# Optimization experiments

Measured on AMD Instinct MI355X. Metric: run time of the kernel, lower is better.

The kernel has to match this reference:

```python
import jax, jax.numpy as jnp
import numpy as np

TEMPERATURE = 8.0  # sqrt(d_k) with d_k = 64
MASK_FILL = -65504.0  # fp16 min, as in the original


def setup_inputs() -> dict:
    key = jax.random.key(0)
    kq, kk, kv, km = jax.random.split(key, 4)
    BH, L, D = 16, 2048, 64
    q = jax.random.normal(kq, (BH, L, D), dtype=jnp.float32)
    k = jax.random.normal(kk, (BH, L, D), dtype=jnp.float32)
    v = jax.random.normal(kv, (BH, L, D), dtype=jnp.float32)
    mask = jax.random.randint(km, (BH, L, L), 0, 2).astype(jnp.bool_)
    return {"q": q, "k": k, "v": v, "mask": mask}


def reference(q, k, v, mask):
    # attn = q @ k^T / temperature, masked_fill, softmax over last dim
    attn = jnp.einsum("bqd,bkd->bqk", q, k) / TEMPERATURE
    attn = jnp.where(mask, MASK_FILL, attn)
    attn = jax.nn.softmax(attn, axis=2)
    # dropout with p=0.0 is identity (eval-mode reference)
    output = jnp.einsum("bqk,bkd->bqd", attn, v)
    return (output, attn)
```

## Files before the change

kernel.cpp:

```cpp
#include <hip/hip_runtime.h>

#define BH 16
#define L 2048
#define D 64
#define QB 64
#define KB 64
#define NKT (L / KB)
#define SCALE 0.125f
#define MASK_FILL -65504.0f

typedef __bf16 bf16x8 __attribute__((ext_vector_type(8)));
typedef float f32x4 __attribute__((ext_vector_type(4)));

__device__ __forceinline__ unsigned f2bf(float f) {
    union { float f; unsigned u; } x; x.f = f;
    return (x.u + 0x7FFFu + ((x.u >> 16) & 1u)) >> 16;
}
__device__ __forceinline__ float bf2f(unsigned short h) {
    union { unsigned u; float f; } x; x.u = ((unsigned)h) << 16;
    return x.f;
}

extern "C" __global__ __launch_bounds__(256)
void prep(const float* __restrict__ k, const float* __restrict__ v,
          const int* __restrict__ mask,
          uint4* __restrict__ wsK, uint4* __restrict__ wsVt,
          unsigned* __restrict__ wsM2)
{
    __shared__ float sT[64 * 68];
    const int b = blockIdx.x;
    const int t = threadIdx.x;

    if (b < 2048) {
        size_t row0 = (size_t)b * 16;
        int lane = t & 63, w4 = t >> 6;
        const int* src = mask + row0 * L;
        unsigned* dst = wsM2 + row0 * 64;
        for (int rr = 0; rr < 4; ++rr) {
            int r = w4 * 4 + rr;
            unsigned word = 0;
            #pragma unroll
            for (int kt = 0; kt < 32; ++kt) {
                int val = __builtin_nontemporal_load(src + (size_t)r * L + kt * 64 + lane);
                word |= (val != 0 ? 1u : 0u) << kt;
            }
            dst[(size_t)r * 64 + lane] = word;
        }
    } else if (b < 3072) {
        int idx = (b - 2048) * 256 + t;
        int c   = idx & 7;
        int key = (idx >> 3) & (L - 1);
        int bh  = idx >> 14;
        const float4* src = (const float4*)(k + ((size_t)(bh * L + key) * D + c * 8));
        float4 a = src[0], bb = src[1];
        uint4 o;
        o.x = f2bf(a.x)  | (f2bf(a.y)  << 16);
        o.y = f2bf(a.z)  | (f2bf(a.w)  << 16);
        o.z = f2bf(bb.x) | (f2bf(bb.y) << 16);
        o.w = f2bf(bb.z) | (f2bf(bb.w) << 16);
        wsK[(size_t)(bh * L + key) * 8 + (c ^ (key & 7))] = o;
    } else {
        int bb = b - 3072;
        int bh = bb >> 5, kt = bb & 31;
        const float4* src = (const float4*)(v + ((size_t)bh * L + kt * 64) * D);
        #pragma unroll
        for (int i = 0; i < 4; ++i) {
            int i4 = i * 256 + t;
            int key = i4 >> 4, c4 = i4 & 15;
            float4 val = src[i4];
            *(float4*)&sT[key * 68 + c4 * 4] = val;
        }
        __syncthreads();
        int d = t >> 2, cg = t & 3;
        #pragma unroll
        for (int j = 0; j < 2; ++j) {
            int c = cg + j * 4;
            unsigned pk[4];
            #pragma unroll
            for (int e = 0; e < 4; ++e) {
                float x0 = sT[(c * 8 + e * 2    ) * 68 + d];
                float x1 = sT[(c * 8 + e * 2 + 1) * 68 + d];
                pk[e] = f2bf(x0) | (f2bf(x1) << 16);
            }
            wsVt[((size_t)(bh * 32 + kt) * 64 + d) * 8 + (c ^ (d & 7))] =
                make_uint4(pk[0], pk[1], pk[2], pk[3]);
        }
    }
}


struct KF { bf16x8 f[8]; };

extern "C" __global__ __launch_bounds__(256, 2)
void sdpa_main(const float* __restrict__ q, const uint4* __restrict__ gKall,
               const uint4* __restrict__ gVall, const unsigned* __restrict__ wsM2,
               float* __restrict__ out, float* __restrict__ attn)
{
    __shared__ unsigned short sP[4][2][16 * 72];

    const int tid = threadIdx.x, lane = tid & 63, w = tid >> 6;
    const int quad = lane >> 4, l15 = lane & 15;
    const int p = blockIdx.x, bh = p & 15, qb = p >> 4;
    const int row0 = qb * QB + w * 16;

    const uint4* gK = gKall + (size_t)bh * L * 8;
    const uint4* gV = gVall + (size_t)bh * L * 8;

    const float* Qp = q + (size_t)(bh * L + row0 + l15) * D + quad * 8;
    float4 qv0 = *(const float4*)(Qp);
    float4 qv1 = *(const float4*)(Qp + 4);
    float4 qv2 = *(const float4*)(Qp + 32);
    float4 qv3 = *(const float4*)(Qp + 36);
    union { bf16x8 v; unsigned short s[8]; } qa0u, qa1u;
    qa0u.s[0] = f2bf(qv0.x * SCALE); qa0u.s[1] = f2bf(qv0.y * SCALE);
    qa0u.s[2] = f2bf(qv0.z * SCALE); qa0u.s[3] = f2bf(qv0.w * SCALE);
    qa0u.s[4] = f2bf(qv1.x * SCALE); qa0u.s[5] = f2bf(qv1.y * SCALE);
    qa0u.s[6] = f2bf(qv1.z * SCALE); qa0u.s[7] = f2bf(qv1.w * SCALE);
    qa1u.s[0] = f2bf(qv2.x * SCALE); qa1u.s[1] = f2bf(qv2.y * SCALE);
    qa1u.s[2] = f2bf(qv2.z * SCALE); qa1u.s[3] = f2bf(qv2.w * SCALE);
    qa1u.s[4] = f2bf(qv3.x * SCALE); qa1u.s[5] = f2bf(qv3.y * SCALE);
    qa1u.s[6] = f2bf(qv3.z * SCALE); qa1u.s[7] = f2bf(qv3.w * SCALE);
    const bf16x8 qa0 = qa0u.v, qa1 = qa1u.v;

    const int s7 = l15 & 7;
    int off[8];
    #pragma unroll
    for (int nt = 0; nt < 4; ++nt) {
        off[nt * 2    ] = (nt * 16 + l15) * 8 + ((quad    ) ^ s7);
        off[nt * 2 + 1] = (nt * 16 + l15) * 8 + ((quad + 4) ^ s7);
    }

    auto loadT = [&](const uint4* base, KF& d) {
        #pragma unroll
        for (int i = 0; i < 8; ++i) d.f[i] = *(const bf16x8*)(base + off[i]);
    };

    const unsigned* Mp = wsM2 + ((size_t)(bh * L) + row0 + quad * 4) * 64 + l15;
    unsigned mb[16];
    #pragma unroll
    for (int r = 0; r < 4; ++r)
        #pragma unroll
        for (int nt = 0; nt < 4; ++nt)
            mb[r * 4 + nt] = Mp[r * 64 + nt * 16];

    float lsum[4] = {0.f, 0.f, 0.f, 0.f};

    KF ka, kb;
    loadT(gK, ka);
    loadT(gK + 512, kb);

    for (int kt = 0; kt < NKT; kt += 2) {
        {
            f32x4 acc[4];
            #pragma unroll
            for (int nt = 0; nt < 4; ++nt) {
                acc[nt] = (f32x4){0.f, 0.f, 0.f, 0.f};
                acc[nt] = __builtin_amdgcn_mfma_f32_16x16x32_bf16(qa0, ka.f[nt*2  ], acc[nt], 0, 0, 0);
                acc[nt] = __builtin_amdgcn_mfma_f32_16x16x32_bf16(qa1, ka.f[nt*2+1], acc[nt], 0, 0, 0);
            }
            if (kt + 2 < NKT) loadT(gK + (size_t)(kt + 2) * 512, ka);
            #pragma unroll
            for (int nt = 0; nt < 4; ++nt)
                #pragma unroll
                for (int r = 0; r < 4; ++r) {
                    float e = __expf(acc[nt][r]);
                    lsum[r] += ((mb[r * 4 + nt] >> kt) & 1u) ? 0.f : e;
                }
        }
        {
            f32x4 acc[4];
            #pragma unroll
            for (int nt = 0; nt < 4; ++nt) {
                acc[nt] = (f32x4){0.f, 0.f, 0.f, 0.f};
                acc[nt] = __builtin_amdgcn_mfma_f32_16x16x32_bf16(qa0, kb.f[nt*2  ], acc[nt], 0, 0, 0);
                acc[nt] = __builtin_amdgcn_mfma_f32_16x16x32_bf16(qa1, kb.f[nt*2+1], acc[nt], 0, 0, 0);
            }
            if (kt + 3 < NKT) loadT(gK + (size_t)(kt + 3) * 512, kb);
            #pragma unroll
            for (int nt = 0; nt < 4; ++nt)
                #pragma unroll
                for (int r = 0; r < 4; ++r) {
                    float e = __expf(acc[nt][r]);
                    lsum[r] += ((mb[r * 4 + nt] >> (kt + 1)) & 1u) ? 0.f : e;
                }
        }
    }

    #pragma unroll
    for (int o = 1; o < 16; o <<= 1)
        #pragma unroll
        for (int r = 0; r < 4; ++r) lsum[r] += __shfl_xor(lsum[r], o, 64);
    float rinv[4];
    #pragma unroll
    for (int r = 0; r < 4; ++r) rinv[r] = 1.0f / lsum[r];

    f32x4 oacc[4];
    #pragma unroll
    for (int d = 0; d < 4; ++d) oacc[d] = (f32x4){0.f, 0.f, 0.f, 0.f};
    float* Ab = attn + ((size_t)bh * L + row0) * L;

    unsigned short* sw0 = &sP[w][0][0];
    unsigned short* sw1 = &sP[w][1][0];

    KF kc, kn, vc;
    loadT(gK, kc);

    for (int kt = 0; kt < NKT; kt += 2) {
        {
            loadT(gV + (size_t)kt * 512, vc);
            f32x4 acc[4];
            #pragma unroll
            for (int nt = 0; nt < 4; ++nt) {
                acc[nt] = (f32x4){0.f, 0.f, 0.f, 0.f};
                acc[nt] = __builtin_amdgcn_mfma_f32_16x16x32_bf16(qa0, kc.f[nt*2  ], acc[nt], 0, 0, 0);
                acc[nt] = __builtin_amdgcn_mfma_f32_16x16x32_bf16(qa1, kc.f[nt*2+1], acc[nt], 0, 0, 0);
            }
            loadT(gK + (size_t)(kt + 1) * 512, kn);
            #pragma unroll
            for (int nt = 0; nt < 4; ++nt)
                #pragma unroll
                for (int r = 0; r < 4; ++r) {
                    float e = __expf(acc[nt][r]);
                    float pr = (((mb[r * 4 + nt] >> kt) & 1u) ? 0.f : e) * rinv[r];
                    const int row = quad * 4 + r;
                    Ab[(size_t)row * L + kt * 64 + nt * 16 + l15] = pr;
                    sw0[row * 72 + nt * 16 + l15] = (unsigned short)f2bf(pr);
                }
            const bf16x8 pa0 = *(const bf16x8*)&sw0[l15 * 72 + quad * 8];
            const bf16x8 pa1 = *(const bf16x8*)&sw0[l15 * 72 + quad * 8 + 32];
            #pragma unroll
            for (int d = 0; d < 4; ++d) {
                oacc[d] = __builtin_amdgcn_mfma_f32_16x16x32_bf16(pa0, vc.f[d*2  ], oacc[d], 0, 0, 0);
                oacc[d] = __builtin_amdgcn_mfma_f32_16x16x32_bf16(pa1, vc.f[d*2+1], oacc[d], 0, 0, 0);
            }
        }
        {
            loadT(gV + (size_t)(kt + 1) * 512, vc);
            f32x4 acc[4];
            #pragma unroll
            for (int nt = 0; nt < 4; ++nt) {
                acc[nt] = (f32x4){0.f, 0.f, 0.f, 0.f};
                acc[nt] = __builtin_amdgcn_mfma_f32_16x16x32_bf16(qa0, kn.f[nt*2  ], acc[nt], 0, 0, 0);
                acc[nt] = __builtin_amdgcn_mfma_f32_16x16x32_bf16(qa1, kn.f[nt*2+1], acc[nt], 0, 0, 0);
            }
            if (kt + 2 < NKT) loadT(gK + (size_t)(kt + 2) * 512, kc);
            #pragma unroll
            for (int nt = 0; nt < 4; ++nt)
                #pragma unroll
                for (int r = 0; r < 4; ++r) {
                    float e = __expf(acc[nt][r]);
                    float pr = (((mb[r * 4 + nt] >> (kt + 1)) & 1u) ? 0.f : e) * rinv[r];
                    const int row = quad * 4 + r;
                    Ab[(size_t)row * L + (kt + 1) * 64 + nt * 16 + l15] = pr;
                    sw1[row * 72 + nt * 16 + l15] = (unsigned short)f2bf(pr);
                }
            const bf16x8 pa0 = *(const bf16x8*)&sw1[l15 * 72 + quad * 8];
            const bf16x8 pa1 = *(const bf16x8*)&sw1[l15 * 72 + quad * 8 + 32];
            #pragma unroll
            for (int d = 0; d < 4; ++d) {
                oacc[d] = __builtin_amdgcn_mfma_f32_16x16x32_bf16(pa0, vc.f[d*2  ], oacc[d], 0, 0, 0);
                oacc[d] = __builtin_amdgcn_mfma_f32_16x16x32_bf16(pa1, vc.f[d*2+1], oacc[d], 0, 0, 0);
            }
        }
    }

    float* Ob = out + ((size_t)bh * L + row0) * D;
    #pragma unroll
    for (int d = 0; d < 4; ++d)
        #pragma unroll
        for (int r = 0; r < 4; ++r)
            Ob[(size_t)(quad * 4 + r) * D + d * 16 + l15] = oacc[d][r];
}


extern "C" __global__ __launch_bounds__(256, 2)
void sdpa_kernel(const float* __restrict__ q, const float* __restrict__ k,
                 const float* __restrict__ v, const int* __restrict__ mask,
                 float* __restrict__ out, float* __restrict__ attn)
{
    __shared__ unsigned short fQ[64 * 72];
    __shared__ unsigned short fK[64 * 72];
    __shared__ unsigned short fVt[64 * 72];
    __shared__ unsigned short fP[64 * 72];
    __shared__ unsigned long long fM[64 * 33];

    const int tid  = threadIdx.x;
    const int lane = tid & 63;
    const int w    = tid >> 6;
    const int quad = lane >> 4;
    const int l15  = lane & 15;

    const int p  = blockIdx.x;
    const int bh = p & (BH - 1);
    const int qb = p >> 4;
    const int q0 = qb * 64;

    const size_t base = (size_t)bh * L * D;
    const float* Qb = q + base + (size_t)q0 * D;
    const float* Kb = k + base;
    const float* Vb = v + base;
    const int*   Mb = mask + (size_t)bh * L * L + (size_t)q0 * L;
    float*       Ab = attn + (size_t)bh * L * L + (size_t)q0 * L;
    float*       Ob = out  + base + (size_t)q0 * D;

    {
        const float2* Qs = (const float2*)Qb;
        for (int i = 0; i < 8; ++i) {
            int idx = i * 256 + tid;
            int row = idx >> 5, d2 = idx & 31;
            float2 val = Qs[idx];
            unsigned pk = f2bf(val.x) | (f2bf(val.y) << 16);
            *(unsigned*)&fQ[row * 72 + d2 * 2] = pk;
        }
    }
    for (int rr = 0; rr < 16; ++rr) {
        int row = w * 16 + rr;
        const int4* Ms = (const int4*)(Mb + (size_t)row * L);
        for (int it = 0; it < 8; ++it) {
            int4 mv = Ms[it * 64 + lane];
            unsigned long long b0 = __ballot(mv.x != 0);
            unsigned long long b1 = __ballot(mv.y != 0);
            unsigned long long b2 = __ballot(mv.z != 0);
            unsigned long long b3 = __ballot(mv.w != 0);
            if (lane == 0) {
                unsigned long long* dst = &fM[row * 33 + it * 4];
                dst[0] = b0; dst[1] = b1; dst[2] = b2; dst[3] = b3;
            }
        }
    }
    __syncthreads();

    const int qrow = w * 16 + l15;
    bf16x8 qa0 = *(const bf16x8*)&fQ[qrow * 72 + quad * 8];
    bf16x8 qa1 = *(const bf16x8*)&fQ[qrow * 72 + quad * 8 + 32];

    float lsum[4] = {0.f, 0.f, 0.f, 0.f};
    for (int kt = 0; kt < 32; ++kt) {
        const int k0 = kt * 64;
        __syncthreads();
        {
            const float2* Ks = (const float2*)(Kb + (size_t)k0 * D);
            for (int i = 0; i < 8; ++i) {
                int idx = i * 256 + tid;
                int row = idx >> 5, d2 = idx & 31;
                float2 val = Ks[idx];
                unsigned pk = f2bf(val.x) | (f2bf(val.y) << 16);
                *(unsigned*)&fK[row * 72 + d2 * 2] = pk;
            }
        }
        __syncthreads();
        f32x4 acc[4];
        for (int nt = 0; nt < 4; ++nt) {
            bf16x8 b0 = *(const bf16x8*)&fK[(nt * 16 + l15) * 72 + quad * 8];
            bf16x8 b1 = *(const bf16x8*)&fK[(nt * 16 + l15) * 72 + quad * 8 + 32];
            f32x4 c = {0.f, 0.f, 0.f, 0.f};
            c = __builtin_amdgcn_mfma_f32_16x16x32_bf16(qa0, b0, c, 0, 0, 0);
            c = __builtin_amdgcn_mfma_f32_16x16x32_bf16(qa1, b1, c, 0, 0, 0);
            acc[nt] = c;
        }
        const int widx = (k0 >> 8) * 4 + (lane & 3);
        const int bsh0 = (k0 >> 2) + (l15 >> 2);
        for (int r = 0; r < 4; ++r) {
            int row = w * 16 + quad * 4 + r;
            unsigned long long mwv = fM[row * 33 + widx];
            float s = 0.f;
            for (int nt = 0; nt < 4; ++nt) {
                float val = acc[nt][r] * SCALE;
                int bit = (int)((mwv >> ((bsh0 + nt * 4) & 63)) & 1ull);
                val = bit ? MASK_FILL : val;
                s += __expf(val);
            }
            lsum[r] += s;
        }
    }
    for (int off = 1; off < 16; off <<= 1)
        for (int r = 0; r < 4; ++r) lsum[r] += __shfl_xor(lsum[r], off, 64);
    float rinv[4];
    for (int r = 0; r < 4; ++r) rinv[r] = 1.0f / lsum[r];

    f32x4 oacc[4];
    for (int nt = 0; nt < 4; ++nt) oacc[nt] = (f32x4){0.f, 0.f, 0.f, 0.f};

    for (int kt = 0; kt < 32; ++kt) {
        const int k0 = kt * 64;
        __syncthreads();
        {
            const float2* Ks = (const float2*)(Kb + (size_t)k0 * D);
            for (int i = 0; i < 8; ++i) {
                int idx = i * 256 + tid;
                int row = idx >> 5, d2 = idx & 31;
                float2 val = Ks[idx];
                unsigned pk = f2bf(val.x) | (f2bf(val.y) << 16);
                *(unsigned*)&fK[row * 72 + d2 * 2] = pk;
            }
        }
        {
            unsigned pk[8];
            for (int jj = 0; jj < 16; ++jj) {
                float val = Vb[(size_t)(k0 + w * 16 + jj) * D + lane];
                unsigned bv = f2bf(val);
                if (jj & 1) pk[jj >> 1] |= bv << 16;
                else        pk[jj >> 1]  = bv;
            }
            uint4* dst = (uint4*)&fVt[lane * 72 + w * 16];
            dst[0] = make_uint4(pk[0], pk[1], pk[2], pk[3]);
            dst[1] = make_uint4(pk[4], pk[5], pk[6], pk[7]);
        }
        __syncthreads();
        f32x4 acc[4];
        for (int nt = 0; nt < 4; ++nt) {
            bf16x8 b0 = *(const bf16x8*)&fK[(nt * 16 + l15) * 72 + quad * 8];
            bf16x8 b1 = *(const bf16x8*)&fK[(nt * 16 + l15) * 72 + quad * 8 + 32];
            f32x4 c = {0.f, 0.f, 0.f, 0.f};
            c = __builtin_amdgcn_mfma_f32_16x16x32_bf16(qa0, b0, c, 0, 0, 0);
            c = __builtin_amdgcn_mfma_f32_16x16x32_bf16(qa1, b1, c, 0, 0, 0);
            acc[nt] = c;
        }
        const int widx = (k0 >> 8) * 4 + (lane & 3);
        const int bsh0 = (k0 >> 2) + (l15 >> 2);
        for (int r = 0; r < 4; ++r) {
            int row = w * 16 + quad * 4 + r;
            unsigned long long mwv = fM[row * 33 + widx];
            for (int nt = 0; nt < 4; ++nt) {
                float val = acc[nt][r] * SCALE;
                int bit = (int)((mwv >> ((bsh0 + nt * 4) & 63)) & 1ull);
                val = bit ? MASK_FILL : val;
                float pr = __expf(val) * rinv[r];
                fP[row * 72 + nt * 16 + l15] = (unsigned short)f2bf(pr);
            }
        }
        for (int it = 0; it < 4; ++it) {
            int row = w * 16 + it * 4 + quad;
            unsigned long long pv = *(const unsigned long long*)&fP[row * 72 + l15 * 4];
            float4 o;
            o.x = bf2f((unsigned short)(pv         & 0xFFFF));
            o.y = bf2f((unsigned short)((pv >> 16) & 0xFFFF));
            o.z = bf2f((unsigned short)((pv >> 32) & 0xFFFF));
            o.w = bf2f((unsigned short)((pv >> 48) & 0xFFFF));
            *(float4*)&Ab[(size_t)row * L + k0 + l15 * 4] = o;
        }
        {
            bf16x8 pa0 = *(const bf16x8*)&fP[qrow * 72 + quad * 8];
            bf16x8 pa1 = *(const bf16x8*)&fP[qrow * 72 + quad * 8 + 32];
            for (int nt = 0; nt < 4; ++nt) {
                bf16x8 vb0 = *(const bf16x8*)&fVt[(nt * 16 + l15) * 72 + quad * 8];
                bf16x8 vb1 = *(const bf16x8*)&fVt[(nt * 16 + l15) * 72 + quad * 8 + 32];
                oacc[nt] = __builtin_amdgcn_mfma_f32_16x16x32_bf16(pa0, vb0, oacc[nt], 0, 0, 0);
                oacc[nt] = __builtin_amdgcn_mfma_f32_16x16x32_bf16(pa1, vb1, oacc[nt], 0, 0, 0);
            }
        }
    }
    for (int nt = 0; nt < 4; ++nt)
        for (int r = 0; r < 4; ++r)
            Ob[(size_t)(w * 16 + quad * 4 + r) * D + nt * 16 + l15] = oacc[nt][r];
}


extern "C" void kernel_launch(void* const* d_in, const int* in_sizes, int n_in,
                              void* d_out, int out_size, void* d_ws, size_t ws_size,
                              hipStream_t stream)
{
    const float* q    = (const float*)d_in[0];
    const float* k    = (const float*)d_in[1];
    const float* v    = (const float*)d_in[2];
    const int*   mask = (const int*)d_in[3];
    float* out  = (float*)d_out;
    float* attn = out + (size_t)BH * L * D;

    const size_t WS_K  = 0;
    const size_t WS_VT = (size_t)BH * L * D * 2;
    const size_t WS_M  = WS_VT + (size_t)BH * L * D * 2;
    const size_t NEED  = WS_M + (size_t)BH * L * 64 * 4;

    if (ws_size >= NEED) {
        uint4* wsK  = (uint4*)((char*)d_ws + WS_K);
        uint4* wsVt = (uint4*)((char*)d_ws + WS_VT);
        unsigned* wsM2 = (unsigned*)((char*)d_ws + WS_M);
        hipLaunchKernelGGL(prep, dim3(3584), dim3(256), 0, stream,
                           k, v, mask, wsK, wsVt, wsM2);
        hipLaunchKernelGGL(sdpa_main, dim3(BH * (L / QB)), dim3(256), 0, stream,
                           q, (const uint4*)wsK, (const uint4*)wsVt, wsM2, out, attn);
    } else {
        hipLaunchKernelGGL(sdpa_kernel, dim3(BH * (L / 64)), dim3(256), 0, stream,
                           q, k, v, mask, out, attn);
    }
}
```

Measured before the change: 506.7 us.

## Fuse mask bit-packing into main kernel via async global-to-LDS staging

Removes the mask-packing phase from the prep kernel. The main attention kernel now streams raw int mask tiles into shared memory with global_load_lds, triple-buffered per wave, and builds the per-row bitmasks during the first (row-sum) pass. The goal is to drop a separate pass that reads the whole mask and writes a packed workspace, and to overlap the mask reads with the QK MFMA work. The trade-offs are extra LDS use, which may limit occupancy, and a hand-coded vmcnt wait whose correctness depends on how many loads are in flight.

```diff
diff --git a/kernel.cpp b/kernel.cpp
--- a/kernel.cpp
+++ b/kernel.cpp
@@ -23,31 +23,14 @@
 
 extern "C" __global__ __launch_bounds__(256)
 void prep(const float* __restrict__ k, const float* __restrict__ v,
-          const int* __restrict__ mask,
-          uint4* __restrict__ wsK, uint4* __restrict__ wsVt,
-          unsigned* __restrict__ wsM2)
+          uint4* __restrict__ wsK, uint4* __restrict__ wsVt)
 {
     __shared__ float sT[64 * 68];
     const int b = blockIdx.x;
     const int t = threadIdx.x;
 
-    if (b < 2048) {
-        size_t row0 = (size_t)b * 16;
-        int lane = t & 63, w4 = t >> 6;
-        const int* src = mask + row0 * L;
-        unsigned* dst = wsM2 + row0 * 64;
-        for (int rr = 0; rr < 4; ++rr) {
-            int r = w4 * 4 + rr;
-            unsigned word = 0;
-            #pragma unroll
-            for (int kt = 0; kt < 32; ++kt) {
-                int val = __builtin_nontemporal_load(src + (size_t)r * L + kt * 64 + lane);
-                word |= (val != 0 ? 1u : 0u) << kt;
-            }
-            dst[(size_t)r * 64 + lane] = word;
-        }
-    } else if (b < 3072) {
-        int idx = (b - 2048) * 256 + t;
+    if (b < 1024) {
+        int idx = b * 256 + t;
         int c   = idx & 7;
         int key = (idx >> 3) & (L - 1);
         int bh  = idx >> 14;
@@ -60,7 +43,7 @@
         o.w = f2bf(bb.z) | (f2bf(bb.w) << 16);
         wsK[(size_t)(bh * L + key) * 8 + (c ^ (key & 7))] = o;
     } else {
-        int bb = b - 3072;
+        int bb = b - 1024;
         int bh = bb >> 5, kt = bb & 31;
         const float4* src = (const float4*)(v + ((size_t)bh * L + kt * 64) * D);
         #pragma unroll
@@ -93,9 +76,10 @@
 
 extern "C" __global__ __launch_bounds__(256, 2)
 void sdpa_main(const float* __restrict__ q, const uint4* __restrict__ gKall,
-               const uint4* __restrict__ gVall, const unsigned* __restrict__ wsM2,
+               const uint4* __restrict__ gVall, const int* __restrict__ mask,
                float* __restrict__ out, float* __restrict__ attn)
 {
+    __shared__ unsigned sM[4][3][16 * 68];
     __shared__ unsigned short sP[4][2][16 * 72];
 
     const int tid = threadIdx.x, lane = tid & 63, w = tid >> 6;
@@ -135,87 +119,90 @@
         for (int i = 0; i < 8; ++i) d.f[i] = *(const bf16x8*)(base + off[i]);
     };
 
-    const unsigned* Mp = wsM2 + ((size_t)(bh * L) + row0 + quad * 4) * 64 + l15;
+    const int* Mraw = mask + ((size_t)bh * L + row0) * L + lane;
+
+    auto stageM = [&](int kt, unsigned* buf) {
+        const int* src = Mraw + kt * 64;
+        #pragma unroll
+        for (int rr = 0; rr < 16; ++rr)
+            __builtin_amdgcn_global_load_lds(
+                (const __attribute__((address_space(1))) unsigned int*)(src + (size_t)rr * L),
+                (__attribute__((address_space(3))) unsigned int*)(buf + rr * 68), 4, 0, 0);
+    };
+
     unsigned mb[16];
     #pragma unroll
-    for (int r = 0; r < 4; ++r)
+    for (int i = 0; i < 16; ++i) mb[i] = 0u;
+
+    float lsum[4] = {0.f, 0.f, 0.f, 0.f};
+
+    unsigned* mbuf0 = &sM[w][0][0];
+    unsigned* mbuf1 = &sM[w][1][0];
+    unsigned* mbuf2 = &sM[w][2][0];
+    stageM(0, mbuf0); stageM(1, mbuf1); stageM(2, mbuf2);
+
+    KF kc, kn;
+    loadT(gK, kc);
+
+    for (int kt = 0; kt < NKT; ++kt) {
+        if (kt + 1 < NKT) loadT(gK + (size_t)(kt + 1) * 512, kn);
+
+        f32x4 acc[4];
+        #pragma unroll
+        for (int nt = 0; nt < 4; ++nt) {
+            acc[nt] = (f32x4){0.f, 0.f, 0.f, 0.f};
+            acc[nt] = __builtin_amdgcn_mfma_f32_16x16x32_bf16(qa0, kc.f[nt*2  ], acc[nt], 0, 0, 0);
+            acc[nt] = __builtin_amdgcn_mfma_f32_16x16x32_bf16(qa1, kc.f[nt*2+1], acc[nt], 0, 0, 0);
+        }
+
+        asm volatile("s_waitcnt vmcnt(32)" ::: "memory");
+
         #pragma unroll
         for (int nt = 0; nt < 4; ++nt)
-            mb[r * 4 + nt] = Mp[r * 64 + nt * 16];
-
-    float lsum[4] = {0.f, 0.f, 0.f, 0.f};
-
-    KF ka, kb;
-    loadT(gK, ka);
-    loadT(gK + 512, kb);
+            #pragma unroll
+            for (int r = 0; r < 4; ++r) {
+                unsigned mv = mbuf0[(quad * 4 + r) * 68 + nt * 16 + l15];
+                unsigned bit = mv ? 1u : 0u;
+                mb[r * 4 + nt] |= bit << kt;
+                float e = __expf(acc[nt][r]);
+                lsum[r] += bit ? 0.f : e;
+            }
+
+        if (kt + 3 < NKT) stageM(kt + 3, mbuf0);
+        unsigned* tmp = mbuf0; mbuf0 = mbuf1; mbuf1 = mbuf2; mbuf2 = tmp;
+        if (kt + 1 < NKT) kc = kn;
+    }
+
+    #pragma unroll
+    for (int o = 1; o < 16; o <<= 1)
+        #pragma unroll
+        for (int r = 0; r < 4; ++r) lsum[r] += __shfl_xor(lsum[r], o, 64);
+    float rinv[4];
+    #pragma unroll
+    for (int r = 0; r < 4; ++r) rinv[r] = 1.0f / lsum[r];
+
+    f32x4 oacc[4];
+    #pragma unroll
+    for (int d = 0; d < 4; ++d) oacc[d] = (f32x4){0.f, 0.f, 0.f, 0.f};
+    float* Ab = attn + ((size_t)bh * L + row0) * L;
+
+    unsigned short* sw0 = &sP[w][0][0];
+    unsigned short* sw1 = &sP[w][1][0];
+
+    KF kc2, kn2, vc;
+    loadT(gK, kc2);
 
     for (int kt = 0; kt < NKT; kt += 2) {
         {
+            loadT(gV + (size_t)kt * 512, vc);
             f32x4 acc[4];
             #pragma unroll
             for (int nt = 0; nt < 4; ++nt) {
                 acc[nt] = (f32x4){0.f, 0.f, 0.f, 0.f};
-                acc[nt] = __builtin_amdgcn_mfma_f32_16x16x32_bf16(qa0, ka.f[nt*2  ], acc[nt], 0, 0, 0);
-                acc[nt] = __builtin_amdgcn_mfma_f32_16x16x32_bf16(qa1, ka.f[nt*2+1], acc[nt], 0, 0, 0);
-            }
-            if (kt + 2 < NKT) loadT(gK + (size_t)(kt + 2) * 512, ka);
-            #pragma unroll
-            for (int nt = 0; nt < 4; ++nt)
-                #pragma unroll
-                for (int r = 0; r < 4; ++r) {
-                    float e = __expf(acc[nt][r]);
-                    lsum[r] += ((mb[r * 4 + nt] >> kt) & 1u) ? 0.f : e;
-                }
-        }
-        {
-            f32x4 acc[4];
-            #pragma unroll
-            for (int nt = 0; nt < 4; ++nt) {
-                acc[nt] = (f32x4){0.f, 0.f, 0.f, 0.f};
-                acc[nt] = __builtin_amdgcn_mfma_f32_16x16x32_bf16(qa0, kb.f[nt*2  ], acc[nt], 0, 0, 0);
-                acc[nt] = __builtin_amdgcn_mfma_f32_16x16x32_bf16(qa1, kb.f[nt*2+1], acc[nt], 0, 0, 0);
-            }
-            if (kt + 3 < NKT) loadT(gK + (size_t)(kt + 3) * 512, kb);
-            #pragma unroll
-            for (int nt = 0; nt < 4; ++nt)
-                #pragma unroll
-                for (int r = 0; r < 4; ++r) {
-                    float e = __expf(acc[nt][r]);
-                    lsum[r] += ((mb[r * 4 + nt] >> (kt + 1)) & 1u) ? 0.f : e;
-                }
-        }
-    }
-
-    #pragma unroll
-    for (int o = 1; o < 16; o <<= 1)
-        #pragma unroll
-        for (int r = 0; r < 4; ++r) lsum[r] += __shfl_xor(lsum[r], o, 64);
-    float rinv[4];
-    #pragma unroll
-    for (int r = 0; r < 4; ++r) rinv[r] = 1.0f / lsum[r];
-
-    f32x4 oacc[4];
-    #pragma unroll
-    for (int d = 0; d < 4; ++d) oacc[d] = (f32x4){0.f, 0.f, 0.f, 0.f};
-    float* Ab = attn + ((size_t)bh * L + row0) * L;
-
-    unsigned short* sw0 = &sP[w][0][0];
-    unsigned short* sw1 = &sP[w][1][0];
-
-    KF kc, kn, vc;
-    loadT(gK, kc);
-
-    for (int kt = 0; kt < NKT; kt += 2) {
-        {
-            loadT(gV + (size_t)kt * 512, vc);
-            f32x4 acc[4];
-            #pragma unroll
-            for (int nt = 0; nt < 4; ++nt) {
-                acc[nt] = (f32x4){0.f, 0.f, 0.f, 0.f};
-                acc[nt] = __builtin_amdgcn_mfma_f32_16x16x32_bf16(qa0, kc.f[nt*2  ], acc[nt], 0, 0, 0);
-                acc[nt] = __builtin_amdgcn_mfma_f32_16x16x32_bf16(qa1, kc.f[nt*2+1], acc[nt], 0, 0, 0);
-            }
-            loadT(gK + (size_t)(kt + 1) * 512, kn);
+                acc[nt] = __builtin_amdgcn_mfma_f32_16x16x32_bf16(qa0, kc2.f[nt*2  ], acc[nt], 0, 0, 0);
+                acc[nt] = __builtin_amdgcn_mfma_f32_16x16x32_bf16(qa1, kc2.f[nt*2+1], acc[nt], 0, 0, 0);
+            }
+            loadT(gK + (size_t)(kt + 1) * 512, kn2);
             #pragma unroll
             for (int nt = 0; nt < 4; ++nt)
                 #pragma unroll
@@ -240,10 +227,10 @@
             #pragma unroll
             for (int nt = 0; nt < 4; ++nt) {
                 acc[nt] = (f32x4){0.f, 0.f, 0.f, 0.f};
-                acc[nt] = __builtin_amdgcn_mfma_f32_16x16x32_bf16(qa0, kn.f[nt*2  ], acc[nt], 0, 0, 0);
-                acc[nt] = __builtin_amdgcn_mfma_f32_16x16x32_bf16(qa1, kn.f[nt*2+1], acc[nt], 0, 0, 0);
-            }
-            if (kt + 2 < NKT) loadT(gK + (size_t)(kt + 2) * 512, kc);
+                acc[nt] = __builtin_amdgcn_mfma_f32_16x16x32_bf16(qa0, kn2.f[nt*2  ], acc[nt], 0, 0, 0);
+                acc[nt] = __builtin_amdgcn_mfma_f32_16x16x32_bf16(qa1, kn2.f[nt*2+1], acc[nt], 0, 0, 0);
+            }
+            if (kt + 2 < NKT) loadT(gK + (size_t)(kt + 2) * 512, kc2);
             #pragma unroll
             for (int nt = 0; nt < 4; ++nt)
                 #pragma unroll
@@ -469,17 +456,15 @@
 
     const size_t WS_K  = 0;
     const size_t WS_VT = (size_t)BH * L * D * 2;
-    const size_t WS_M  = WS_VT + (size_t)BH * L * D * 2;
-    const size_t NEED  = WS_M + (size_t)BH * L * 64 * 4;
+    const size_t NEED  = WS_VT + (size_t)BH * L * D * 2;
 
     if (ws_size >= NEED) {
         uint4* wsK  = (uint4*)((char*)d_ws + WS_K);
         uint4* wsVt = (uint4*)((char*)d_ws + WS_VT);
-        unsigned* wsM2 = (unsigned*)((char*)d_ws + WS_M);
-        hipLaunchKernelGGL(prep, dim3(3584), dim3(256), 0, stream,
-                           k, v, mask, wsK, wsVt, wsM2);
+        hipLaunchKernelGGL(prep, dim3(1536), dim3(256), 0, stream,
+                           k, v, wsK, wsVt);
         hipLaunchKernelGGL(sdpa_main, dim3(BH * (L / QB)), dim3(256), 0, stream,
-                           q, (const uint4*)wsK, (const uint4*)wsVt, wsM2, out, attn);
+                           q, (const uint4*)wsK, (const uint4*)wsVt, mask, out, attn);
     } else {
         hipLaunchKernelGGL(sdpa_kernel, dim3(BH * (L / 64)), dim3(256), 0, stream,
                            q, k, v, mask, out, attn);
```

Measured after the change: 582.7 us. +15.0%, slower.

## Split key range across wave pairs and halve query block per workgroup

Applied to the files above, without the earlier changes.

Each workgroup now covers 32 query rows instead of 64. Pairs of waves split the key tiles in half, combine their partial row sums and output accumulators through shared memory, and use two block barriers to do so. Occupancy is raised to 4 blocks per SM and twice as many blocks are launched, giving more parallelism and latency hiding. In exchange there is extra shared-memory reduction traffic and register pressure under the tighter launch bound, and each K/V tile is reloaded by more blocks.

```diff
diff --git a/kernel.cpp b/kernel.cpp
--- a/kernel.cpp
+++ b/kernel.cpp
@@ -3,7 +3,7 @@
 #define BH 16
 #define L 2048
 #define D 64
-#define QB 64
+#define QB 32
 #define KB 64
 #define NKT (L / KB)
 #define SCALE 0.125f
@@ -91,17 +91,22 @@
 
 struct KF { bf16x8 f[8]; };
 
-extern "C" __global__ __launch_bounds__(256, 2)
+extern "C" __global__ __launch_bounds__(256, 4)
 void sdpa_main(const float* __restrict__ q, const uint4* __restrict__ gKall,
                const uint4* __restrict__ gVall, const unsigned* __restrict__ wsM2,
                float* __restrict__ out, float* __restrict__ attn)
 {
     __shared__ unsigned short sP[4][2][16 * 72];
+    __shared__ float sPart[4][16];
+    __shared__ float sO[2][16][68];
 
     const int tid = threadIdx.x, lane = tid & 63, w = tid >> 6;
+    const int rg = w >> 1, h = w & 1;
     const int quad = lane >> 4, l15 = lane & 15;
     const int p = blockIdx.x, bh = p & 15, qb = p >> 4;
-    const int row0 = qb * QB + w * 16;
+    const int row0 = qb * QB + rg * 16;
+    const int kt0 = h * (NKT / 2);
+    const int ktE = kt0 + (NKT / 2);
 
     const uint4* gK = gKall + (size_t)bh * L * 8;
     const uint4* gV = gVall + (size_t)bh * L * 8;
@@ -146,10 +151,10 @@
     float lsum[4] = {0.f, 0.f, 0.f, 0.f};
 
     KF ka, kb;
-    loadT(gK, ka);
-    loadT(gK + 512, kb);
-
-    for (int kt = 0; kt < NKT; kt += 2) {
+    loadT(gK + (size_t)kt0 * 512, ka);
+    loadT(gK + (size_t)(kt0 + 1) * 512, kb);
+
+    for (int kt = kt0; kt < ktE; kt += 2) {
         {
             f32x4 acc[4];
             #pragma unroll
@@ -158,7 +163,7 @@
                 acc[nt] = __builtin_amdgcn_mfma_f32_16x16x32_bf16(qa0, ka.f[nt*2  ], acc[nt], 0, 0, 0);
                 acc[nt] = __builtin_amdgcn_mfma_f32_16x16x32_bf16(qa1, ka.f[nt*2+1], acc[nt], 0, 0, 0);
             }
-            if (kt + 2 < NKT) loadT(gK + (size_t)(kt + 2) * 512, ka);
+            if (kt + 2 < ktE) loadT(gK + (size_t)(kt + 2) * 512, ka);
             #pragma unroll
             for (int nt = 0; nt < 4; ++nt)
                 #pragma unroll
@@ -175,7 +180,7 @@
                 acc[nt] = __builtin_amdgcn_mfma_f32_16x16x32_bf16(qa0, kb.f[nt*2  ], acc[nt], 0, 0, 0);
                 acc[nt] = __builtin_amdgcn_mfma_f32_16x16x32_bf16(qa1, kb.f[nt*2+1], acc[nt], 0, 0, 0);
             }
-            if (kt + 3 < NKT) loadT(gK + (size_t)(kt + 3) * 512, kb);
+            if (kt + 3 < ktE) loadT(gK + (size_t)(kt + 3) * 512, kb);
             #pragma unroll
             for (int nt = 0; nt < 4; ++nt)
                 #pragma unroll
@@ -190,9 +195,15 @@
     for (int o = 1; o < 16; o <<= 1)
         #pragma unroll
         for (int r = 0; r < 4; ++r) lsum[r] += __shfl_xor(lsum[r], o, 64);
+    if (l15 == 0) {
+        #pragma unroll
+        for (int r = 0; r < 4; ++r) sPart[w][quad * 4 + r] = lsum[r];
+    }
+    __syncthreads();
     float rinv[4];
     #pragma unroll
-    for (int r = 0; r < 4; ++r) rinv[r] = 1.0f / lsum[r];
+    for (int r = 0; r < 4; ++r)
+        rinv[r] = 1.0f / (sPart[rg * 2][quad * 4 + r] + sPart[rg * 2 + 1][quad * 4 + r]);
 
     f32x4 oacc[4];
     #pragma unroll
@@ -202,20 +213,20 @@
     unsigned short* sw0 = &sP[w][0][0];
     unsigned short* sw1 = &sP[w][1][0];
 
-    KF kc, kn, vc;
-    loadT(gK, kc);
-
-    for (int kt = 0; kt < NKT; kt += 2) {
+    KF kc2, kn2, vc;
+    loadT(gK + (size_t)kt0 * 512, kc2);
+
+    for (int kt = kt0; kt < ktE; kt += 2) {
         {
             loadT(gV + (size_t)kt * 512, vc);
             f32x4 acc[4];
             #pragma unroll
             for (int nt = 0; nt < 4; ++nt) {
                 acc[nt] = (f32x4){0.f, 0.f, 0.f, 0.f};
-                acc[nt] = __builtin_amdgcn_mfma_f32_16x16x32_bf16(qa0, kc.f[nt*2  ], acc[nt], 0, 0, 0);
-                acc[nt] = __builtin_amdgcn_mfma_f32_16x16x32_bf16(qa1, kc.f[nt*2+1], acc[nt], 0, 0, 0);
-            }
-            loadT(gK + (size_t)(kt + 1) * 512, kn);
+                acc[nt] = __builtin_amdgcn_mfma_f32_16x16x32_bf16(qa0, kc2.f[nt*2  ], acc[nt], 0, 0, 0);
+                acc[nt] = __builtin_amdgcn_mfma_f32_16x16x32_bf16(qa1, kc2.f[nt*2+1], acc[nt], 0, 0, 0);
+            }
+            loadT(gK + (size_t)(kt + 1) * 512, kn2);
             #pragma unroll
             for (int nt = 0; nt < 4; ++nt)
                 #pragma unroll
@@ -240,10 +251,10 @@
             #pragma unroll
             for (int nt = 0; nt < 4; ++nt) {
                 acc[nt] = (f32x4){0.f, 0.f, 0.f, 0.f};
-                acc[nt] = __builtin_amdgcn_mfma_f32_16x16x32_bf16(qa0, kn.f[nt*2  ], acc[nt], 0, 0, 0);
-                acc[nt] = __builtin_amdgcn_mfma_f32_16x16x32_bf16(qa1, kn.f[nt*2+1], acc[nt], 0, 0, 0);
-            }
-            if (kt + 2 < NKT) loadT(gK + (size_t)(kt + 2) * 512, kc);
+                acc[nt] = __builtin_amdgcn_mfma_f32_16x16x32_bf16(qa0, kn2.f[nt*2  ], acc[nt], 0, 0, 0);
+                acc[nt] = __builtin_amdgcn_mfma_f32_16x16x32_bf16(qa1, kn2.f[nt*2+1], acc[nt], 0, 0, 0);
+            }
+            if (kt + 2 < ktE) loadT(gK + (size_t)(kt + 2) * 512, kc2);
             #pragma unroll
             for (int nt = 0; nt < 4; ++nt)
                 #pragma unroll
@@ -264,12 +275,23 @@
         }
     }
 
-    float* Ob = out + ((size_t)bh * L + row0) * D;
-    #pragma unroll
-    for (int d = 0; d < 4; ++d)
-        #pragma unroll
-        for (int r = 0; r < 4; ++r)
-            Ob[(size_t)(quad * 4 + r) * D + d * 16 + l15] = oacc[d][r];
+    if (h == 1) {
+        #pragma unroll
+        for (int d = 0; d < 4; ++d)
+            #pragma unroll
+            for (int r = 0; r < 4; ++r)
+                sO[rg][quad * 4 + r][d * 16 + l15] = oacc[d][r];
+    }
+    __syncthreads();
+    if (h == 0) {
+        float* Ob = out + ((size_t)bh * L + row0) * D;
+        #pragma unroll
+        for (int d = 0; d < 4; ++d)
+            #pragma unroll
+            for (int r = 0; r < 4; ++r)
+                Ob[(size_t)(quad * 4 + r) * D + d * 16 + l15] =
+                    oacc[d][r] + sO[rg][quad * 4 + r][d * 16 + l15];
+    }
 }
 
 
```

Result: slower. 803.2 us (+58.5%).
